# Kernel tuning notes

Measured on AMD Instinct MI355X. Metric: run time of the kernel, lower is better.

Reference implementation:

```python
import jax, jax.numpy as jnp
import numpy as np
import math


def setup_inputs() -> dict:
    key = jax.random.key(0)
    kq, kk, kv, kt, kd = jax.random.split(key, 5)
    B, L, H, E = 2, 2048, 16, 64
    return {
        "queries": jax.random.normal(kq, (B, L, H, E), dtype=jnp.float32),
        "keys": jax.random.normal(kk, (B, L, H, E), dtype=jnp.float32),
        "values": jax.random.normal(kv, (B, L, H, E), dtype=jnp.float32),
        "tau": jax.random.uniform(kt, (B, 1), dtype=jnp.float32),
        "delta": jax.random.normal(kd, (B, L), dtype=jnp.float32),
    }


def reference(queries, keys, values, tau, delta):
    # queries/keys/values: [B, L, H, E]; tau: [B,1]; delta: [B,S]
    B, L, H, E = queries.shape
    scale = 1.0 / math.sqrt(E)
    # scores: [B, H, L, S]; tau broadcasts [B,1,1,1], delta broadcasts [B,1,1,S]
    scores = (jnp.einsum('blhe,bshe->bhls', queries, keys)
              * tau[:, None, None, :]
              + delta[:, None, None, :])
    # causal mask (mask_flag=True, attn_mask=None path)
    causal = jnp.triu(jnp.ones((L, L), dtype=bool), k=1)
    scores = jnp.where(causal, -jnp.inf, scores)
    A = jax.nn.softmax(scale * scores, axis=-1)  # dropout p=0
    V = jnp.einsum('bhls,bshd->blhd', A, values)
    return V
```

## Files before the change

kernel.cpp:

```cpp
#include <hip/hip_runtime.h>
#include <math.h>

#define LL 2048
#define HH 16
#define EE 64
#define ROWSTR (HH*EE)
#define NBH 32
#define NT 16
#define NST 32
#define SCALE 0.125f
#define LOG2E 1.4426950408889634f
#define TILE_SH 4096
#define KPRE_OFF 4096
#define TILES_TOTAL ((size_t)NBH * NST)
#define WS_NEED (16384ull + 2ull * TILES_TOTAL * TILE_SH * 2ull)

using bf16x8 = __attribute__((ext_vector_type(8))) __bf16;
using f32x4  = __attribute__((ext_vector_type(4))) float;
using s16x4  = __attribute__((ext_vector_type(4))) short;

__device__ __forceinline__ unsigned pkbf(float lo, float hi) {
    unsigned l = __builtin_bit_cast(unsigned, lo) + 0x8000u;
    unsigned h = __builtin_bit_cast(unsigned, hi) + 0x8000u;
    return __builtin_amdgcn_perm(h, l, 0x07060302u);
}
__device__ __forceinline__ uint4 pack8(float4 a, float4 b) {
    uint4 u; u.x = pkbf(a.x, a.y); u.y = pkbf(a.z, a.w);
    u.z = pkbf(b.x, b.y); u.w = pkbf(b.z, b.w); return u;
}

#if __has_builtin(__builtin_amdgcn_mfma_f32_16x16x16_bf16)
using bf16x4 = __attribute__((ext_vector_type(4))) __bf16;
__device__ __forceinline__ f32x4 mfma16(s16x4 a, s16x4 b, f32x4 c) {
    return __builtin_amdgcn_mfma_f32_16x16x16_bf16(
        __builtin_bit_cast(bf16x4, a), __builtin_bit_cast(bf16x4, b), c, 0, 0, 0);
}
#else
__device__ __forceinline__ f32x4 mfma16(s16x4 a, s16x4 b, f32x4 c) {
    return __builtin_amdgcn_mfma_f32_16x16x16bf16_1k(a, b, c, 0, 0, 0);
}
#endif

__device__ __forceinline__ void gl_lds16(const void* g, void* l) {
    __builtin_amdgcn_global_load_lds(
        (const __attribute__((address_space(1))) unsigned int*)(unsigned long long)g,
        (__attribute__((address_space(3))) unsigned int*)(unsigned long long)l,
        16, 0, 0);
}

__global__ __launch_bounds__(256) void dsprep(
    const float* __restrict__ K, const float* __restrict__ V,
    const float* __restrict__ delta, float* __restrict__ ws)
{
    const int bid = blockIdx.x;
    const int t = threadIdx.x;
    float* dsc = ws;
    unsigned short* kpre = (unsigned short*)(ws + KPRE_OFF);
    unsigned short* vpre = kpre + TILES_TOTAL * TILE_SH;

    if (bid >= NBH * NST) {
        const int i = (bid - NBH * NST) * 256 + t;
        dsc[i] = delta[i] * (SCALE * LOG2E);
        return;
    }
    const int bh = bid & 31, st = bid >> 5;
    const int b = bh >> 4, h = bh & 15;

    unsigned short* kimg = kpre + ((size_t)bh * NST + st) * TILE_SH;
    #pragma unroll
    for (int i = 0; i < 2; ++i) {
        const int slot = t + i * 256;
        const int k = slot >> 3, c = slot & 7;
        const float* src = K + ((size_t)(b * LL + st * 64 + k) * HH + h) * EE + c * 8;
        float4 a = ((const float4*)src)[0], bq = ((const float4*)src)[1];
        *(uint4*)&kimg[k * 64 + (c ^ (k & 7)) * 8] = pack8(a, bq);
    }

    __shared__ float vt[64 * 65];
    {
        const int s = t >> 2, seg = (t & 3) * 16;
        const float* src = V + ((size_t)(b * LL + st * 64 + s) * HH + h) * EE + seg;
        #pragma unroll
        for (int i = 0; i < 4; ++i) {
            float4 f = ((const float4*)src)[i];
            vt[s * 65 + seg + 4 * i + 0] = f.x;
            vt[s * 65 + seg + 4 * i + 1] = f.y;
            vt[s * 65 + seg + 4 * i + 2] = f.z;
            vt[s * 65 + seg + 4 * i + 3] = f.w;
        }
    }
    __syncthreads();
    {
        unsigned short* vimg = vpre + ((size_t)bh * NST + st) * TILE_SH;
        const int e = t >> 2, g = t & 3;
        unsigned u[8];
        #pragma unroll
        for (int A = 0; A < 4; ++A) {
            float x0 = vt[(16 * A + 4 * g + 0) * 65 + e];
            float x1 = vt[(16 * A + 4 * g + 1) * 65 + e];
            float x2 = vt[(16 * A + 4 * g + 2) * 65 + e];
            float x3 = vt[(16 * A + 4 * g + 3) * 65 + e];
            u[2 * A]     = pkbf(x0, x1);
            u[2 * A + 1] = pkbf(x2, x3);
        }
        *(uint4*)&vimg[e * 64 + ((2 * g)     ^ (e & 7)) * 8] = uint4{u[0], u[1], u[2], u[3]};
        *(uint4*)&vimg[e * 64 + ((2 * g + 1) ^ (e & 7)) * 8] = uint4{u[4], u[5], u[6], u[7]};
    }
}

__global__ __launch_bounds__(512, 4) void dsattn_dma(
    const float* __restrict__ Qg, const float* __restrict__ taug,
    const float* __restrict__ ws_, float* __restrict__ Og)
{
    __shared__ __align__(16) unsigned short Ks[2][TILE_SH];
    __shared__ __align__(16) unsigned short Vt[2][TILE_SH];

    const int tid  = threadIdx.x;
    const int w    = tid >> 6;
    const int lane = tid & 63;
    const int m    = lane & 15;
    const int quad = lane >> 4;

    const int bid = blockIdx.x;
    const int bh  = bid & (NBH - 1);
    const int g   = bid >> 5;
    const int tt  = (g < 8) ? (15 - g) : (g - 8);
    const int b   = bh >> 4;
    const int h   = bh & 15;

    const float* dsc = ws_;
    const unsigned short* kpre = (const unsigned short*)(ws_ + KPRE_OFF);
    const unsigned short* vpre = kpre + TILES_TOTAL * TILE_SH;
    const unsigned short* ktiles = kpre + (size_t)bh * NST * TILE_SH;
    const unsigned short* vtiles = vpre + (size_t)bh * NST * TILE_SH;

    const float qscale = taug[b] * (SCALE * LOG2E);
    const int diag_st = 2 * tt + (w >> 2);
    const int thr = (w & 3) * 16 + m - quad * 4;

    bf16x8 qb[2];
    {
        const float* qp = Qg + ((size_t)(b * LL + tt * 128 + w * 16 + m) * HH + h) * EE + quad * 8;
        #pragma unroll
        for (int ch = 0; ch < 2; ++ch) {
            float4 f0 = *(const float4*)(qp + ch * 32);
            float4 f1 = *(const float4*)(qp + ch * 32 + 4);
            f0.x *= qscale; f0.y *= qscale; f0.z *= qscale; f0.w *= qscale;
            f1.x *= qscale; f1.y *= qscale; f1.z *= qscale; f1.w *= qscale;
            qb[ch] = __builtin_bit_cast(bf16x8, pack8(f0, f1));
        }
    }

    const int nst = 2 * tt + 2;
    const float* dbase = dsc + b * LL + quad * 4;

    gl_lds16(ktiles + tid * 8, &Ks[0][w * 512]);
    gl_lds16(vtiles + tid * 8, &Vt[0][w * 512]);

    f32x4 Oacc[4] = {};
    float l_ = 0.f;

    for (int st = 0; st < nst; ++st) {
        const int par = st & 1;
        const unsigned short* KsP = Ks[par];
        const unsigned short* VtP = Vt[par];

        __syncthreads();

        if (st + 1 < nst) {
            gl_lds16(ktiles + (st + 1) * TILE_SH + tid * 8, &Ks[par ^ 1][w * 512]);
            gl_lds16(vtiles + (st + 1) * TILE_SH + tid * 8, &Vt[par ^ 1][w * 512]);
        }

        if (st <= diag_st) {
            const float* dp = dbase + st * 64;
            float4 dr0 = *(const float4*)(dp);
            float4 dr1 = *(const float4*)(dp + 16);
            float4 dr2 = *(const float4*)(dp + 32);
            float4 dr3 = *(const float4*)(dp + 48);

            f32x4 S[4];
            S[0] = __builtin_bit_cast(f32x4, dr0);
            S[1] = __builtin_bit_cast(f32x4, dr1);
            S[2] = __builtin_bit_cast(f32x4, dr2);
            S[3] = __builtin_bit_cast(f32x4, dr3);
            #pragma unroll
            for (int n = 0; n < 4; ++n) {
                bf16x8 kf = *(const bf16x8*)&KsP[(16 * n + m) * 64 + (quad ^ (m & 7)) * 8];
                S[n] = __builtin_amdgcn_mfma_f32_16x16x32_bf16(kf, qb[0], S[n], 0, 0, 0);
            }
            #pragma unroll
            for (int n = 0; n < 4; ++n) {
                bf16x8 kf = *(const bf16x8*)&KsP[(16 * n + m) * 64 + ((quad + 4) ^ (m & 7)) * 8];
                S[n] = __builtin_amdgcn_mfma_f32_16x16x32_bf16(kf, qb[1], S[n], 0, 0, 0);
            }

            if (st == diag_st) {
                #pragma unroll
                for (int n = 0; n < 4; ++n)
                    #pragma unroll
                    for (int r = 0; r < 4; ++r)
                        if (16 * n + r > thr) S[n][r] = -INFINITY;
            }

            float rs[4];
            #pragma unroll
            for (int n = 0; n < 4; ++n) {
                float p0 = __builtin_amdgcn_exp2f(S[n][0]);
                float p1 = __builtin_amdgcn_exp2f(S[n][1]);
                float p2 = __builtin_amdgcn_exp2f(S[n][2]);
                float p3 = __builtin_amdgcn_exp2f(S[n][3]);
                S[n][0] = p0; S[n][1] = p1; S[n][2] = p2; S[n][3] = p3;
                rs[n] = (p0 + p1) + (p2 + p3);
            }
            l_ += (rs[0] + rs[1]) + (rs[2] + rs[3]);

            s16x4 pb[4];
            #pragma unroll
            for (int n = 0; n < 4; ++n) {
                uint2 u; u.x = pkbf(S[n][0], S[n][1]); u.y = pkbf(S[n][2], S[n][3]);
                pb[n] = __builtin_bit_cast(s16x4, u);
            }

            #pragma unroll
            for (int eb = 0; eb < 4; ++eb) {
                const int e = 16 * eb + m;
                uint4 r0 = *(const uint4*)&VtP[e * 64 + ((2 * quad)     ^ (m & 7)) * 8];
                uint4 r1 = *(const uint4*)&VtP[e * 64 + ((2 * quad + 1) ^ (m & 7)) * 8];
                f32x4 o = Oacc[eb];
                o = mfma16(__builtin_bit_cast(s16x4, uint2{r0.x, r0.y}), pb[0], o);
                o = mfma16(__builtin_bit_cast(s16x4, uint2{r0.z, r0.w}), pb[1], o);
                o = mfma16(__builtin_bit_cast(s16x4, uint2{r1.x, r1.y}), pb[2], o);
                o = mfma16(__builtin_bit_cast(s16x4, uint2{r1.z, r1.w}), pb[3], o);
                Oacc[eb] = o;
            }
        }
    }

    {
        float lt = l_ + __shfl_xor(l_, 16);
        lt = lt + __shfl_xor(lt, 32);
        const float inv = __builtin_amdgcn_rcpf(lt);
        float* op = Og + ((size_t)(b * LL + tt * 128 + w * 16 + m) * HH + h) * EE + quad * 4;
        #pragma unroll
        for (int n = 0; n < 4; ++n) {
            float4 o = {Oacc[n][0] * inv, Oacc[n][1] * inv, Oacc[n][2] * inv, Oacc[n][3] * inv};
            *(float4*)(op + 16 * n) = o;
        }
    }
}

__global__ __launch_bounds__(512, 4) void dsattn_reg(
    const float* __restrict__ Qg, const float* __restrict__ Kg,
    const float* __restrict__ Vg, const float* __restrict__ taug,
    const float* __restrict__ dg, float* __restrict__ Og)
{
    __shared__ __align__(16) unsigned short Ks[2][64 * 64];
    __shared__ __align__(16) unsigned short Vt[2][64 * 64];

    const int tid  = threadIdx.x;
    const int w    = tid >> 6;
    const int lane = tid & 63;
    const int m    = lane & 15;
    const int quad = lane >> 4;

    const int bid = blockIdx.x;
    const int bh  = bid & (NBH - 1);
    const int g   = bid >> 5;
    const int tt  = (g < 8) ? (15 - g) : (g - 8);
    const int b   = bh >> 4;
    const int h   = bh & 15;

    const float qscale = taug[b] * (SCALE * LOG2E);
    const float dscale = SCALE * LOG2E;
    const int diag_st = 2 * tt + (w >> 2);
    const int thr = (w & 3) * 16 + m - quad * 4;

    bf16x8 qb[2];
    {
        const float* qp = Qg + ((size_t)(b * LL + tt * 128 + w * 16 + m) * HH + h) * EE + quad * 8;
        #pragma unroll
        for (int ch = 0; ch < 2; ++ch) {
            float4 f0 = *(const float4*)(qp + ch * 32);
            float4 f1 = *(const float4*)(qp + ch * 32 + 4);
            f0.x *= qscale; f0.y *= qscale; f0.z *= qscale; f0.w *= qscale;
            f1.x *= qscale; f1.y *= qscale; f1.z *= qscale; f1.w *= qscale;
            qb[ch] = __builtin_bit_cast(bf16x8, pack8(f0, f1));
        }
    }

    const int skey = tid >> 3, kc = tid & 7, se0 = (tid & 7) * 8;
    const int sv = (tid & 31) * 2, ve = (tid >> 5) * 4;
    const float* kbase = Kg + ((size_t)b * LL * HH + h) * EE;
    const float* vbase = Vg + ((size_t)b * LL * HH + h) * EE;
    const float* dbase = dg + b * LL;
    const int nst = 2 * tt + 2;

    float4 kr0, kr1, va, vb, dr0, dr1, dr2, dr3;
    {
        const float* kp = kbase + (size_t)skey * ROWSTR + se0;
        kr0 = ((const float4*)kp)[0]; kr1 = ((const float4*)kp)[1];
        const float* vp = vbase + (size_t)sv * ROWSTR + ve;
        va = *(const float4*)(vp); vb = *(const float4*)(vp + ROWSTR);
        const float* dp = dbase + quad * 4;
        dr0 = *(const float4*)(dp); dr1 = *(const float4*)(dp + 16);
        dr2 = *(const float4*)(dp + 32); dr3 = *(const float4*)(dp + 48);
    }

    f32x4 Oacc[4] = {};
    float l_ = 0.f;

    for (int st = 0; st < nst; ++st) {
        const int par = st & 1;
        unsigned short* KsP = Ks[par];
        unsigned short* VtP = Vt[par];

        *(uint4*)&KsP[skey * 64 + (kc ^ (skey & 7)) * 8] = pack8(kr0, kr1);
        {
            float ra[4] = {va.x, va.y, va.z, va.w};
            float rb[4] = {vb.x, vb.y, vb.z, vb.w};
            #pragma unroll
            for (int i = 0; i < 4; ++i) {
                const int e = ve + i;
                *(unsigned*)&VtP[e * 64 + (((sv >> 3) ^ (e & 7)) * 8) + (sv & 7)] = pkbf(ra[i], rb[i]);
            }
        }
        __syncthreads();

        f32x4 dvx[4];
        dvx[0] = f32x4{dr0.x * dscale, dr0.y * dscale, dr0.z * dscale, dr0.w * dscale};
        dvx[1] = f32x4{dr1.x * dscale, dr1.y * dscale, dr1.z * dscale, dr1.w * dscale};
        dvx[2] = f32x4{dr2.x * dscale, dr2.y * dscale, dr2.z * dscale, dr2.w * dscale};
        dvx[3] = f32x4{dr3.x * dscale, dr3.y * dscale, dr3.z * dscale, dr3.w * dscale};

        if (st + 1 < nst) {
            const int row = (st + 1) * 64;
            const float* kp = kbase + (size_t)(row + skey) * ROWSTR + se0;
            kr0 = ((const float4*)kp)[0]; kr1 = ((const float4*)kp)[1];
            const float* vp = vbase + (size_t)(row + sv) * ROWSTR + ve;
            va = *(const float4*)(vp); vb = *(const float4*)(vp + ROWSTR);
            const float* dp = dbase + row + quad * 4;
            dr0 = *(const float4*)(dp); dr1 = *(const float4*)(dp + 16);
            dr2 = *(const float4*)(dp + 32); dr3 = *(const float4*)(dp + 48);
        }

        if (st <= diag_st) {
            f32x4 S[4];
            #pragma unroll
            for (int n = 0; n < 4; ++n) {
                bf16x8 kf = *(const bf16x8*)&KsP[(16 * n + m) * 64 + (quad ^ (m & 7)) * 8];
                S[n] = __builtin_amdgcn_mfma_f32_16x16x32_bf16(kf, qb[0], dvx[n], 0, 0, 0);
            }
            #pragma unroll
            for (int n = 0; n < 4; ++n) {
                bf16x8 kf = *(const bf16x8*)&KsP[(16 * n + m) * 64 + ((quad + 4) ^ (m & 7)) * 8];
                S[n] = __builtin_amdgcn_mfma_f32_16x16x32_bf16(kf, qb[1], S[n], 0, 0, 0);
            }
            if (st == diag_st) {
                #pragma unroll
                for (int n = 0; n < 4; ++n)
                    #pragma unroll
                    for (int r = 0; r < 4; ++r)
                        if (16 * n + r > thr) S[n][r] = -INFINITY;
            }
            float rs[4];
            #pragma unroll
            for (int n = 0; n < 4; ++n) {
                float p0 = __builtin_amdgcn_exp2f(S[n][0]);
                float p1 = __builtin_amdgcn_exp2f(S[n][1]);
                float p2 = __builtin_amdgcn_exp2f(S[n][2]);
                float p3 = __builtin_amdgcn_exp2f(S[n][3]);
                S[n][0] = p0; S[n][1] = p1; S[n][2] = p2; S[n][3] = p3;
                rs[n] = (p0 + p1) + (p2 + p3);
            }
            l_ += (rs[0] + rs[1]) + (rs[2] + rs[3]);

            s16x4 pb[4];
            #pragma unroll
            for (int n = 0; n < 4; ++n) {
                uint2 u; u.x = pkbf(S[n][0], S[n][1]); u.y = pkbf(S[n][2], S[n][3]);
                pb[n] = __builtin_bit_cast(s16x4, u);
            }
            #pragma unroll
            for (int eb = 0; eb < 4; ++eb) {
                const int e = 16 * eb + m;
                s16x4 vf[4];
                #pragma unroll
                for (int n = 0; n < 4; ++n)
                    vf[n] = *(const s16x4*)&VtP[e * 64 + (((2 * n + (quad >> 1)) ^ (m & 7)) * 8) + (quad & 1) * 4];
                #pragma unroll
                for (int n = 0; n < 4; ++n)
                    Oacc[eb] = mfma16(vf[n], pb[n], Oacc[eb]);
            }
        }
    }

    {
        float lt = l_ + __shfl_xor(l_, 16);
        lt = lt + __shfl_xor(lt, 32);
        const float inv = __builtin_amdgcn_rcpf(lt);
        float* op = Og + ((size_t)(b * LL + tt * 128 + w * 16 + m) * HH + h) * EE + quad * 4;
        #pragma unroll
        for (int n = 0; n < 4; ++n) {
            float4 o = {Oacc[n][0] * inv, Oacc[n][1] * inv, Oacc[n][2] * inv, Oacc[n][3] * inv};
            *(float4*)(op + 16 * n) = o;
        }
    }
}

extern "C" void kernel_launch(void* const* d_in, const int* in_sizes, int n_in,
                              void* d_out, int out_size, void* d_ws, size_t ws_size,
                              hipStream_t stream) {
    const float* Q     = (const float*)d_in[0];
    const float* K     = (const float*)d_in[1];
    const float* V     = (const float*)d_in[2];
    const float* tau   = (const float*)d_in[3];
    const float* delta = (const float*)d_in[4];
    float* out = (float*)d_out;
    float* ws  = (float*)d_ws;
    if (ws_size >= WS_NEED) {
        dsprep<<<dim3(NBH * NST + 16), dim3(256), 0, stream>>>(K, V, delta, ws);
        dsattn_dma<<<dim3(NBH * NT), dim3(512), 0, stream>>>(Q, tau, ws, out);
    } else {
        dsattn_reg<<<dim3(NBH * NT), dim3(512), 0, stream>>>(Q, K, V, tau, delta, out);
    }
}
```

Before: 135.4 us.

## Shrink attention blocks to 64 query rows with 256 threads, doubling grid size

The DMA attention kernel moves from 128-query-row blocks of 512 threads to 64-row blocks of 256 threads, giving 1024 blocks ordered longest-first by query tile. Each thread now issues two async global-to-LDS copies per K and V tile, and the per-wave diagonal skip logic is removed because every wave in a block shares the same diagonal tile. This aims to improve load balance across the causal triangle and raise occupancy. The cost is twice the K/V tile traffic per query row and more barriers per unit of work.

After: 127.4 us. -5.9%, faster.

```diff
diff --git a/kernel.cpp b/kernel.cpp
--- a/kernel.cpp
+++ b/kernel.cpp
@@ -6,7 +6,7 @@
 #define EE 64
 #define ROWSTR (HH*EE)
 #define NBH 32
-#define NT 16
+#define NQT 32
 #define NST 32
 #define SCALE 0.125f
 #define LOG2E 1.4426950408889634f
@@ -108,7 +108,7 @@
     }
 }
 
-__global__ __launch_bounds__(512, 4) void dsattn_dma(
+__global__ __launch_bounds__(256, 8) void dsattn_dma(
     const float* __restrict__ Qg, const float* __restrict__ taug,
     const float* __restrict__ ws_, float* __restrict__ Og)
 {
@@ -123,8 +123,7 @@
 
     const int bid = blockIdx.x;
     const int bh  = bid & (NBH - 1);
-    const int g   = bid >> 5;
-    const int tt  = (g < 8) ? (15 - g) : (g - 8);
+    const int qt  = (NQT - 1) - (bid >> 5);
     const int b   = bh >> 4;
     const int h   = bh & 15;
 
@@ -135,12 +134,11 @@
     const unsigned short* vtiles = vpre + (size_t)bh * NST * TILE_SH;
 
     const float qscale = taug[b] * (SCALE * LOG2E);
-    const int diag_st = 2 * tt + (w >> 2);
-    const int thr = (w & 3) * 16 + m - quad * 4;
+    const int thr = w * 16 + m - quad * 4;
 
     bf16x8 qb[2];
     {
-        const float* qp = Qg + ((size_t)(b * LL + tt * 128 + w * 16 + m) * HH + h) * EE + quad * 8;
+        const float* qp = Qg + ((size_t)(b * LL + qt * 64 + w * 16 + m) * HH + h) * EE + quad * 8;
         #pragma unroll
         for (int ch = 0; ch < 2; ++ch) {
             float4 f0 = *(const float4*)(qp + ch * 32);
@@ -151,89 +149,88 @@
         }
     }
 
-    const int nst = 2 * tt + 2;
     const float* dbase = dsc + b * LL + quad * 4;
 
-    gl_lds16(ktiles + tid * 8, &Ks[0][w * 512]);
-    gl_lds16(vtiles + tid * 8, &Vt[0][w * 512]);
+    gl_lds16(ktiles + tid * 8,        &Ks[0][w * 512]);
+    gl_lds16(ktiles + 2048 + tid * 8, &Ks[0][2048 + w * 512]);
+    gl_lds16(vtiles + tid * 8,        &Vt[0][w * 512]);
+    gl_lds16(vtiles + 2048 + tid * 8, &Vt[0][2048 + w * 512]);
 
     f32x4 Oacc[4] = {};
     float l_ = 0.f;
 
-    for (int st = 0; st < nst; ++st) {
+    for (int st = 0; st <= qt; ++st) {
         const int par = st & 1;
         const unsigned short* KsP = Ks[par];
         const unsigned short* VtP = Vt[par];
 
         __syncthreads();
 
-        if (st + 1 < nst) {
-            gl_lds16(ktiles + (st + 1) * TILE_SH + tid * 8, &Ks[par ^ 1][w * 512]);
-            gl_lds16(vtiles + (st + 1) * TILE_SH + tid * 8, &Vt[par ^ 1][w * 512]);
-        }
-
-        if (st <= diag_st) {
-            const float* dp = dbase + st * 64;
-            float4 dr0 = *(const float4*)(dp);
-            float4 dr1 = *(const float4*)(dp + 16);
-            float4 dr2 = *(const float4*)(dp + 32);
-            float4 dr3 = *(const float4*)(dp + 48);
-
-            f32x4 S[4];
-            S[0] = __builtin_bit_cast(f32x4, dr0);
-            S[1] = __builtin_bit_cast(f32x4, dr1);
-            S[2] = __builtin_bit_cast(f32x4, dr2);
-            S[3] = __builtin_bit_cast(f32x4, dr3);
-            #pragma unroll
-            for (int n = 0; n < 4; ++n) {
-                bf16x8 kf = *(const bf16x8*)&KsP[(16 * n + m) * 64 + (quad ^ (m & 7)) * 8];
-                S[n] = __builtin_amdgcn_mfma_f32_16x16x32_bf16(kf, qb[0], S[n], 0, 0, 0);
-            }
-            #pragma unroll
-            for (int n = 0; n < 4; ++n) {
-                bf16x8 kf = *(const bf16x8*)&KsP[(16 * n + m) * 64 + ((quad + 4) ^ (m & 7)) * 8];
-                S[n] = __builtin_amdgcn_mfma_f32_16x16x32_bf16(kf, qb[1], S[n], 0, 0, 0);
-            }
-
-            if (st == diag_st) {
+        if (st < qt) {
+            const unsigned short* kn = ktiles + (st + 1) * TILE_SH;
+            const unsigned short* vn = vtiles + (st + 1) * TILE_SH;
+            gl_lds16(kn + tid * 8,        &Ks[par ^ 1][w * 512]);
+            gl_lds16(kn + 2048 + tid * 8, &Ks[par ^ 1][2048 + w * 512]);
+            gl_lds16(vn + tid * 8,        &Vt[par ^ 1][w * 512]);
+            gl_lds16(vn + 2048 + tid * 8, &Vt[par ^ 1][2048 + w * 512]);
+        }
+
+        const float* dp = dbase + st * 64;
+        f32x4 S[4];
+        S[0] = __builtin_bit_cast(f32x4, *(const float4*)(dp));
+        S[1] = __builtin_bit_cast(f32x4, *(const float4*)(dp + 16));
+        S[2] = __builtin_bit_cast(f32x4, *(const float4*)(dp + 32));
+        S[3] = __builtin_bit_cast(f32x4, *(const float4*)(dp + 48));
+
+        #pragma unroll
+        for (int n = 0; n < 4; ++n) {
+            bf16x8 kf = *(const bf16x8*)&KsP[(16 * n + m) * 64 + (quad ^ (m & 7)) * 8];
+            S[n] = __builtin_amdgcn_mfma_f32_16x16x32_bf16(kf, qb[0], S[n], 0, 0, 0);
+        }
+        #pragma unroll
+        for (int n = 0; n < 4; ++n) {
+            bf16x8 kf = *(const bf16x8*)&KsP[(16 * n + m) * 64 + ((quad + 4) ^ (m & 7)) * 8];
+            S[n] = __builtin_amdgcn_mfma_f32_16x16x32_bf16(kf, qb[1], S[n], 0, 0, 0);
+        }
+
+        if (st == qt) {
+            #pragma unroll
+            for (int n = 0; n < 4; ++n)
                 #pragma unroll
-                for (int n = 0; n < 4; ++n)
-                    #pragma unroll
-                    for (int r = 0; r < 4; ++r)
-                        if (16 * n + r > thr) S[n][r] = -INFINITY;
-            }
-
-            float rs[4];
-            #pragma unroll
-            for (int n = 0; n < 4; ++n) {
-                float p0 = __builtin_amdgcn_exp2f(S[n][0]);
-                float p1 = __builtin_amdgcn_exp2f(S[n][1]);
-                float p2 = __builtin_amdgcn_exp2f(S[n][2]);
-                float p3 = __builtin_amdgcn_exp2f(S[n][3]);
-                S[n][0] = p0; S[n][1] = p1; S[n][2] = p2; S[n][3] = p3;
-                rs[n] = (p0 + p1) + (p2 + p3);
-            }
-            l_ += (rs[0] + rs[1]) + (rs[2] + rs[3]);
-
-            s16x4 pb[4];
-            #pragma unroll
-            for (int n = 0; n < 4; ++n) {
-                uint2 u; u.x = pkbf(S[n][0], S[n][1]); u.y = pkbf(S[n][2], S[n][3]);
-                pb[n] = __builtin_bit_cast(s16x4, u);
-            }
-
-            #pragma unroll
-            for (int eb = 0; eb < 4; ++eb) {
-                const int e = 16 * eb + m;
-                uint4 r0 = *(const uint4*)&VtP[e * 64 + ((2 * quad)     ^ (m & 7)) * 8];
-                uint4 r1 = *(const uint4*)&VtP[e * 64 + ((2 * quad + 1) ^ (m & 7)) * 8];
-                f32x4 o = Oacc[eb];
-                o = mfma16(__builtin_bit_cast(s16x4, uint2{r0.x, r0.y}), pb[0], o);
-                o = mfma16(__builtin_bit_cast(s16x4, uint2{r0.z, r0.w}), pb[1], o);
-                o = mfma16(__builtin_bit_cast(s16x4, uint2{r1.x, r1.y}), pb[2], o);
-                o = mfma16(__builtin_bit_cast(s16x4, uint2{r1.z, r1.w}), pb[3], o);
-                Oacc[eb] = o;
-            }
+                for (int r = 0; r < 4; ++r)
+                    if (16 * n + r > thr) S[n][r] = -INFINITY;
+        }
+
+        float rs[4];
+        #pragma unroll
+        for (int n = 0; n < 4; ++n) {
+            float p0 = __builtin_amdgcn_exp2f(S[n][0]);
+            float p1 = __builtin_amdgcn_exp2f(S[n][1]);
+            float p2 = __builtin_amdgcn_exp2f(S[n][2]);
+            float p3 = __builtin_amdgcn_exp2f(S[n][3]);
+            S[n][0] = p0; S[n][1] = p1; S[n][2] = p2; S[n][3] = p3;
+            rs[n] = (p0 + p1) + (p2 + p3);
+        }
+        l_ += (rs[0] + rs[1]) + (rs[2] + rs[3]);
+
+        s16x4 pb[4];
+        #pragma unroll
+        for (int n = 0; n < 4; ++n) {
+            uint2 u; u.x = pkbf(S[n][0], S[n][1]); u.y = pkbf(S[n][2], S[n][3]);
+            pb[n] = __builtin_bit_cast(s16x4, u);
+        }
+
+        #pragma unroll
+        for (int eb = 0; eb < 4; ++eb) {
+            const int e = 16 * eb + m;
+            uint4 r0 = *(const uint4*)&VtP[e * 64 + ((2 * quad)     ^ (m & 7)) * 8];
+            uint4 r1 = *(const uint4*)&VtP[e * 64 + ((2 * quad + 1) ^ (m & 7)) * 8];
+            f32x4 o = Oacc[eb];
+            o = mfma16(__builtin_bit_cast(s16x4, uint2{r0.x, r0.y}), pb[0], o);
+            o = mfma16(__builtin_bit_cast(s16x4, uint2{r0.z, r0.w}), pb[1], o);
+            o = mfma16(__builtin_bit_cast(s16x4, uint2{r1.x, r1.y}), pb[2], o);
+            o = mfma16(__builtin_bit_cast(s16x4, uint2{r1.z, r1.w}), pb[3], o);
+            Oacc[eb] = o;
         }
     }
 
@@ -241,7 +238,7 @@
         float lt = l_ + __shfl_xor(l_, 16);
         lt = lt + __shfl_xor(lt, 32);
         const float inv = __builtin_amdgcn_rcpf(lt);
-        float* op = Og + ((size_t)(b * LL + tt * 128 + w * 16 + m) * HH + h) * EE + quad * 4;
+        float* op = Og + ((size_t)(b * LL + qt * 64 + w * 16 + m) * HH + h) * EE + quad * 4;
         #pragma unroll
         for (int n = 0; n < 4; ++n) {
             float4 o = {Oacc[n][0] * inv, Oacc[n][1] * inv, Oacc[n][2] * inv, Oacc[n][3] * inv};
@@ -420,8 +417,8 @@
     float* ws  = (float*)d_ws;
     if (ws_size >= WS_NEED) {
         dsprep<<<dim3(NBH * NST + 16), dim3(256), 0, stream>>>(K, V, delta, ws);
-        dsattn_dma<<<dim3(NBH * NT), dim3(512), 0, stream>>>(Q, tau, ws, out);
+        dsattn_dma<<<dim3(NBH * NQT), dim3(256), 0, stream>>>(Q, tau, ws, out);
     } else {
-        dsattn_reg<<<dim3(NBH * NT), dim3(512), 0, stream>>>(Q, K, V, tau, delta, out);
-    }
-}
+        dsattn_reg<<<dim3(NBH * (NQT / 2)), dim3(512), 0, stream>>>(Q, K, V, tau, delta, out);
+    }
+}
```
